# Kernel tuning notes

Measured on AMD Instinct MI355X. Metric: run time of the kernel, lower is better.

## Reference

```python
import jax, jax.numpy as jnp
import numpy as np

Cl, Nl, Cv, Nv, M = 32, 128, 8, 64, 500000


def _sample1d(line, g):
    # line: [C, N]; g in [-1,1]; align_corners=True, zeros padding
    C, N = line.shape
    ix = (g + 1.0) * 0.5 * (N - 1)
    i0 = jnp.floor(ix)
    w = ix - i0
    i0 = i0.astype(jnp.int32)
    def gth(i, wt):
        valid = (i >= 0) & (i < N)
        return line[:, jnp.clip(i, 0, N - 1)] * (wt * valid)
    return (gth(i0, 1.0 - w) + gth(i0 + 1, w)).T  # [M, C]


def _sample2d(plane, gx, gy):
    # plane: [C, H, W]; grid x -> W axis, y -> H axis (torch grid_sample convention)
    C, H, W = plane.shape
    ix = (gx + 1.0) * 0.5 * (W - 1)
    iy = (gy + 1.0) * 0.5 * (H - 1)
    x0 = jnp.floor(ix); y0 = jnp.floor(iy)
    wx = ix - x0; wy = iy - y0
    x0 = x0.astype(jnp.int32); y0 = y0.astype(jnp.int32)
    flat = plane.reshape(C, -1)
    def gth(xi, yi, wt):
        valid = (xi >= 0) & (xi < W) & (yi >= 0) & (yi < H)
        idx = jnp.clip(yi, 0, H - 1) * W + jnp.clip(xi, 0, W - 1)
        return flat[:, idx] * (wt * valid)
    out = (gth(x0, y0, (1 - wx) * (1 - wy)) + gth(x0 + 1, y0, wx * (1 - wy))
           + gth(x0, y0 + 1, (1 - wx) * wy) + gth(x0 + 1, y0 + 1, wx * wy))
    return out.T  # [M, C]


def _sample3d(vol, gx, gy, gz):
    # vol: [C, D, H, W]; grid (x,y,z) -> (W,H,D) axes
    C, D, H, W = vol.shape
    ix = (gx + 1.0) * 0.5 * (W - 1)
    iy = (gy + 1.0) * 0.5 * (H - 1)
    iz = (gz + 1.0) * 0.5 * (D - 1)
    x0 = jnp.floor(ix); y0 = jnp.floor(iy); z0 = jnp.floor(iz)
    wx = ix - x0; wy = iy - y0; wz = iz - z0
    x0 = x0.astype(jnp.int32); y0 = y0.astype(jnp.int32); z0 = z0.astype(jnp.int32)
    flat = vol.reshape(C, -1)
    out = 0.0
    for dz in (0, 1):
        for dy in (0, 1):
            for dx in (0, 1):
                xi, yi, zi = x0 + dx, y0 + dy, z0 + dz
                wt = ((wx if dx else 1 - wx) * (wy if dy else 1 - wy) * (wz if dz else 1 - wz))
                valid = (xi >= 0) & (xi < W) & (yi >= 0) & (yi < H) & (zi >= 0) & (zi < D)
                idx = (jnp.clip(zi, 0, D - 1) * H + jnp.clip(yi, 0, H - 1)) * W + jnp.clip(xi, 0, W - 1)
                out = out + flat[:, idx] * (wt * valid)
    return out.T  # [M, C]


def setup_inputs() -> dict:
    key = jax.random.key(0)
    ks = jax.random.split(key, 16)
    rng, shift = 0.4, 0.1
    coordinates = jax.random.uniform(ks[0], (1, M, 3), minval=-1.0, maxval=1.0)
    line_x = jax.random.uniform(ks[1], (Cl, Nl)) * rng + shift
    line_y = jax.random.uniform(ks[2], (Cl, Nl)) * rng + shift
    line_z = jax.random.uniform(ks[3], (Cl, Nl)) * rng + shift
    plane_xy = jax.random.normal(ks[4], (Cl, Nl, Nl)) * rng + shift
    plane_yz = jax.random.normal(ks[5], (Cl, Nl, Nl)) * rng + shift
    plane_xz = jax.random.normal(ks[6], (Cl, Nl, Nl)) * rng + shift
    volume = jax.random.normal(ks[7], (Cv, Nv, Nv, Nv)) * rng + shift
    def lin(k, fi, fo):
        k1, k2 = jax.random.split(k)
        lim = 1.0 / np.sqrt(fi)
        return (jax.random.uniform(k1, (fi, fo), minval=-lim, maxval=lim),
                jax.random.uniform(k2, (fo,), minval=-lim, maxval=lim))
    Wx, bx = lin(ks[8], Cl, Cl)
    Wy, by = lin(ks[9], Cl, Cl)
    Wz, bz = lin(ks[10], Cl, Cl)
    W1, b1 = lin(ks[11], Cl + Cv, 128)
    W2, b2 = lin(ks[12], 128, 1)
    return dict(coordinates=coordinates, line_x=line_x, line_y=line_y, line_z=line_z,
                plane_xy=plane_xy, plane_yz=plane_yz, plane_xz=plane_xz, volume=volume,
                Wx=Wx, bx=bx, Wy=Wy, by=by, Wz=Wz, bz=bz, W1=W1, b1=b1, W2=W2, b2=b2)


def reference(coordinates, line_x, line_y, line_z, plane_xy, plane_yz, plane_xz, volume,
              Wx, bx, Wy, by, Wz, bz, W1, b1, W2, b2):
    c = coordinates[0]  # [M, 3], batch squeezed like the torch code
    x, y, z = c[:, 0], c[:, 1], c[:, 2]
    x_e = _sample1d(line_x, x)
    y_e = _sample1d(line_y, y)
    z_e = _sample1d(line_z, z)
    xy_e = _sample2d(plane_xy, x, y)
    yz_e = _sample2d(plane_yz, y, z)
    xz_e = _sample2d(plane_xz, x, z)
    xyz_e = _sample3d(volume, x, y, z)
    phi = lambda e, W, b: jax.nn.relu(e) @ W + b  # Sequential(ReLU, Linear)
    yztran = phi(yz_e, Wx, bx)
    xztran = phi(xz_e, Wy, by)
    xytran = phi(xy_e, Wz, bz)
    xtran = phi(x_e, Wx, bx)
    ytran = phi(y_e, Wy, by)
    ztran = phi(z_e, Wz, bz)
    features = xtran * yztran + ytran * xztran + ztran * xytran
    features = jnp.concatenate([features, xyz_e], axis=-1)  # [M, Cl+Cv]
    h = jax.nn.relu(features @ W1 + b1)
    return h @ W2 + b2  # [M, 1]
```

## Files before the change

### kernel.cpp

```cpp
#include <hip/hip_runtime.h>

typedef unsigned short u16;
typedef u16 u16x8 __attribute__((ext_vector_type(8)));
typedef _Float16 half2 __attribute__((ext_vector_type(2)));
typedef _Float16 h8v __attribute__((ext_vector_type(8)));
typedef float f4v __attribute__((ext_vector_type(4)));

union H8 { h8v v; half2 p[4]; };

static __device__ __forceinline__ float bf2f(u16 u) {
    union { unsigned int i; float f; } v;
    v.i = ((unsigned int)u) << 16;
    return v.f;
}
static __device__ __forceinline__ u16 f2bf(float f) {
    union { float f; unsigned int i; } v;
    v.f = f;
    unsigned int x = v.i;
    x += 0x7fffu + ((x >> 16) & 1u);
    return (u16)(x >> 16);
}
static __device__ __forceinline__ float gld(int dt, const void* p, int i) {
    return dt ? ((const float*)p)[i] : bf2f(((const u16*)p)[i]);
}
static __device__ __forceinline__ int detect_dt(const void* coords) {
    u16 v = ((const u16*)coords)[threadIdx.x & 63];
    int e = (v >> 7) & 0xFF;
    bool inr = (e >= 90) && (e <= 126);
    unsigned long long m = __ballot(inr);
    return (__popcll(m) >= 56) ? 0 : 1;
}
static __device__ __forceinline__ half2 pk(float a, float b) {
    return __builtin_bit_cast(half2, __builtin_amdgcn_cvt_pkrtz(a, b));
}

static __device__ __forceinline__ void wave_lds_fence() {
    __threadfence_block();
}

#define WF_OFF        64u
#define PLANES_S_OFF  34304u
#define VOL_S_OFF     3180032u
#define LINES_S_OFF   7374336u
#define PART_OFF      7398912u
#define TOT_OFF       9496064u
#define ORDER_OFF     9512448u

#define NBUCK 4096
#define HBLOCKS 256


static __device__ __forceinline__ int make_key3(float x, float y, float z) {
    int kx = min(max((int)((x + 1.0f) * 8.0f), 0), 15);
    int ky = min(max((int)((y + 1.0f) * 8.0f), 0), 15);
    int kz = min(max((int)((z + 1.0f) * 8.0f), 0), 15);
    return (kz * 16 + ky) * 16 + kx;
}
static __device__ __forceinline__ int make_key(int dt, const void* coords, int p) {
    return make_key3(gld(dt, coords, p * 3 + 0), gld(dt, coords, p * 3 + 1),
                     gld(dt, coords, p * 3 + 2));
}

static __device__ __forceinline__ void weights_work(
    int dt, int r,
    const void* Wx, const void* bx, const void* Wy, const void* by,
    const void* Wz, const void* bz, const void* W1, const void* b1,
    const void* W2, const void* b2, float* wbase)
{
    _Float16* WtH = (_Float16*)wbase;
    float*    bv  = wbase + 1536;
    _Float16* W1H = (_Float16*)(wbase + 1632);
    float*    b1v = wbase + 5728;
    float*    W2v = wbase + 5856;
    float*    b2v = wbase + 5984;
    if (r < 3072) {
        int m = r >> 10, idx = r & 1023;
        int o = idx >> 5, c = idx & 31;
        const void* s = (m == 0) ? Wx : (m == 1) ? Wy : Wz;
        WtH[r] = (_Float16)gld(dt, s, c * 32 + o);
    } else if (r < 3168) {
        int q2 = r - 3072;
        int m = q2 >> 5, c = q2 & 31;
        const void* s = (m == 0) ? bx : (m == 1) ? by : bz;
        bv[q2] = gld(dt, s, c);
    } else if (r < 11360) {
        int idx = r - 3168;
        int j = idx >> 6, i = idx & 63;
        W1H[idx] = (i < 40) ? (_Float16)gld(dt, W1, i * 128 + j) : (_Float16)0.0f;
    } else if (r < 11488) {
        b1v[r - 11360] = gld(dt, b1, r - 11360);
    } else if (r < 11616) {
        W2v[r - 11488] = gld(dt, W2, r - 11488);
    } else if (r == 11616) {
        b2v[0] = gld(dt, b2, 0);
    }
}

__global__ __launch_bounds__(256) void kp_prep_all(
    const void* __restrict__ coords,
    const void* __restrict__ lx, const void* __restrict__ ly,
    const void* __restrict__ lz,
    const void* __restrict__ pxy, const void* __restrict__ pyz,
    const void* __restrict__ pxz, const void* __restrict__ vol,
// ... 88 lines not shown
    }
    psum[t] = s;
    __syncthreads();
    if (t == 0) {
        unsigned int run = 0;
        for (int i = 0; i < 256; ++i) { unsigned int v = psum[i]; psum[i] = run; run += v; }
    }
    __syncthreads();
    unsigned int run = psum[t];
#pragma unroll
    for (int i = 0; i < 16; ++i) {
        int bkt = t * 16 + i;
        cnt[bkt] = run + (unsigned int)part[b * NBUCK + bkt];
        run += bs[i];
    }
    __syncthreads();
    int dt = detect_dt(coords);
    const u16* cu = (const u16*)coords;
    for (int p = b * 256 + t; p < M; p += HBLOCKS * 256) {
        float x = gld(dt, coords, p * 3 + 0);
        float y = gld(dt, coords, p * 3 + 1);
        float z = gld(dt, coords, p * 3 + 2);
        int key = make_key3(x, y, z);
        unsigned int pos = atomicAdd(&cnt[key], 1u);
        order[pos] = p;
        if (dt == 0) {
            scoords[pos * 3 + 0] = cu[p * 3 + 0];
            scoords[pos * 3 + 1] = cu[p * 3 + 1];
            scoords[pos * 3 + 2] = cu[p * 3 + 2];
        }
    }
}

struct Samp { int i0, i1; float w0, w1; };

static __device__ __forceinline__ Samp make_samp(float g, int N) {
    float ix = (g + 1.0f) * 0.5f * (float)(N - 1);
    float fl = floorf(ix);
    float w  = ix - fl;
    int i  = (int)fl;
    int i1 = i + 1;
    float v0 = (i  >= 0 && i  < N) ? 1.0f : 0.0f;
    float v1 = (i1 >= 0 && i1 < N) ? 1.0f : 0.0f;
    Samp s;
    s.w0 = (1.0f - w) * v0;
    s.w1 = w * v1;
    s.i0 = min(max(i, 0), N - 1);
    s.i1 = min(max(i1, 0), N - 1);
    return s;
}

#define MFMA16(a, b, c) __builtin_amdgcn_mfma_f32_16x16x32_f16((a), (b), (c), 0, 0, 0)

#define SRE 40
#define SR2 72

static __device__ __forceinline__ void term_mfma(
    int lane, const u16* __restrict__ Ls, const Samp& sl,
    const u16* __restrict__ Ps, const Samp& sa, const Samp& sb,
    const _Float16* __restrict__ Wt, const float* __restrict__ bvt,
    _Float16* El, _Float16* Ep, float (&feat)[4][2][4])
{
    int q = lane >> 4, l15 = lane & 15;
    const u16x8* l0  = (const u16x8*)(Ls + sl.i0 * 32);
    const u16x8* l1  = (const u16x8*)(Ls + sl.i1 * 32);
    const u16x8* p00 = (const u16x8*)(Ps + (sb.i0 * 128 + sa.i0) * 32);
    const u16x8* p01 = (const u16x8*)(Ps + (sb.i0 * 128 + sa.i1) * 32);
    const u16x8* p10 = (const u16x8*)(Ps + (sb.i1 * 128 + sa.i0) * 32);
    const u16x8* p11 = (const u16x8*)(Ps + (sb.i1 * 128 + sa.i1) * 32);
    float w00 = sb.w0 * sa.w0, w01 = sb.w0 * sa.w1;
    float w10 = sb.w1 * sa.w0, w11 = sb.w1 * sa.w1;
#pragma unroll
    for (int cc = 0; cc < 4; ++cc) {
        u16x8 A0 = l0[cc], A1 = l1[cc];
        u16x8 Q00 = p00[cc], Q01 = p01[cc], Q10 = p10[cc], Q11 = p11[cc];
        H8 hl, hp;
#pragma unroll
        for (int kk = 0; kk < 4; ++kk) {
            int k0 = 2 * kk, k1 = k0 + 1;
            float el0 = sl.w0 * bf2f(A0[k0]) + sl.w1 * bf2f(A1[k0]);
            float el1 = sl.w0 * bf2f(A0[k1]) + sl.w1 * bf2f(A1[k1]);
            float ep0 = w00 * bf2f(Q00[k0]) + w01 * bf2f(Q01[k0])
                      + w10 * bf2f(Q10[k0]) + w11 * bf2f(Q11[k0]);
            float ep1 = w00 * bf2f(Q00[k1]) + w01 * bf2f(Q01[k1])
                      + w10 * bf2f(Q10[k1]) + w11 * bf2f(Q11[k1]);
            hl.p[kk] = pk(fmaxf(el0, 0.0f), fmaxf(el1, 0.0f));
            hp.p[kk] = pk(fmaxf(ep0, 0.0f), fmaxf(ep1, 0.0f));
        }
        *(h8v*)&El[lane * SRE + cc * 8] = hl.v;
        *(h8v*)&Ep[lane * SRE + cc * 8] = hp.v;
    }
    wave_lds_fence();
    h8v bf0 = *(const h8v*)&Wt[(l15) * 32 + q * 8];
    h8v bf1 = *(const h8v*)&Wt[(16 + l15) * 32 + q * 8];
    float bb0 = bvt[l15], bb1 = bvt[16 + l15];
    f4v c0 = {bb0, bb0, bb0, bb0};
    f4v c1 = {bb1, bb1, bb1, bb1};
#pragma unroll
    for (int mt = 0; mt < 4; ++mt) {
        h8v aL = *(const h8v*)&El[(mt * 16 + l15) * SRE + q * 8];
        h8v aP = *(const h8v*)&Ep[(mt * 16 + l15) * SRE + q * 8];
        f4v ta0 = MFMA16(aL, bf0, c0);
        f4v tb0 = MFMA16(aP, bf0, c0);
        f4v ta1 = MFMA16(aL, bf1, c1);
        f4v tb1 = MFMA16(aP, bf1, c1);
#pragma unroll
        for (int r = 0; r < 4; ++r) {
            feat[mt][0][r] += ta0[r] * tb0[r];
            feat[mt][1][r] += ta1[r] * tb1[r];
        }
    }
    wave_lds_fence();
}

__global__ __launch_bounds__(64) void kp_main_mfma(
    const void* __restrict__ coords, const int* __restrict__ order,
    const u16* __restrict__ scoords,
    const u16* __restrict__ planes_s, const u16* __restrict__ vol_s,
    const u16* __restrict__ lines_s,
    const float* __restrict__ wbase,
    void* __restrict__ out, int M)
{
    __shared__ _Float16 eb[5120];
    __shared__ float res[64];
    int dt = detect_dt(coords);
    const _Float16* WtH = (const _Float16*)wbase;
    const float*    bv  = wbase + 1536;
    const _Float16* W1H = (const _Float16*)(wbase + 1632);
    const float*    b1v = wbase + 5728;
    const float*    W2v = wbase + 5856;
    const float*    b2v = wbase + 5984;

    int lane = threadIdx.x;
    int q = lane >> 4, l15 = lane & 15;
    _Float16* El = eb;
    _Float16* Ep = eb + 2560;
    _Float16* E2 = eb;

    int p = blockIdx.x * 64 + lane;
    p = min(p, M - 1);
    int sp = order[p];

    float x, y, z;
    if (dt == 0) {
        x = bf2f(scoords[p * 3 + 0]);
        y = bf2f(scoords[p * 3 + 1]);
        z = bf2f(scoords[p * 3 + 2]);
    } else {
        x = ((const float*)coords)[sp * 3 + 0];
        y = ((const float*)coords)[sp * 3 + 1];
        z = ((const float*)coords)[sp * 3 + 2];
    }

    Samp sx = make_samp(x, 128), sy = make_samp(y, 128), sz = make_samp(z, 128);

    float feat[4][2][4];
#pragma unroll
    for (int mt = 0; mt < 4; ++mt)
#pragma unroll
        for (int n = 0; n < 2; ++n)
#pragma unroll
            for (int r = 0; r < 4; ++r) feat[mt][n][r] = 0.0f;

    term_mfma(lane, lines_s + 0 * 4096, sx, planes_s + 1 * 524288, sy, sz,
              WtH + 0,    bv + 0,  El, Ep, feat);
    term_mfma(lane, lines_s + 1 * 4096, sy, planes_s + 2 * 524288, sx, sz,
              WtH + 1024, bv + 32, El, Ep, feat);
    term_mfma(lane, lines_s + 2 * 4096, sz, planes_s + 0 * 524288, sx, sy,
              WtH + 2048, bv + 64, El, Ep, feat);

#pragma unroll
    for (int mt = 0; mt < 4; ++mt)
#pragma unroll
        for (int n = 0; n < 2; ++n)
#pragma unroll
            for (int r = 0; r < 4; ++r)
                E2[(mt * 16 + q * 4 + r) * SR2 + n * 16 + l15] =
                    (_Float16)feat[mt][n][r];
    {
        Samp vx = make_samp(x, 64), vy = make_samp(y, 64), vz = make_samp(z, 64);
        float vf[8];
#pragma unroll
        for (int c = 0; c < 8; ++c) vf[c] = 0.0f;
#pragma unroll
        for (int corner = 0; corner < 8; ++corner) {
            int dx = corner & 1, dy = (corner >> 1) & 1, dz = corner >> 2;
            int xi = dx ? vx.i1 : vx.i0;
            int yi = dy ? vy.i1 : vy.i0;
            int zi = dz ? vz.i1 : vz.i0;
            float w = (dx ? vx.w1 : vx.w0) * (dy ? vy.w1 : vy.w0) * (dz ? vz.w1 : vz.w0);
            u16x8 v = *(const u16x8*)(vol_s + (((zi * 64) + yi) * 64 + xi) * 8);
#pragma unroll
            for (int c = 0; c < 8; ++c)
                vf[c] = fmaf(w, bf2f(v[c]), vf[c]);
        }
        H8 hv;
#pragma unroll
        for (int k = 0; k < 4; ++k) hv.p[k] = pk(vf[2 * k], vf[2 * k + 1]);
        *(h8v*)&E2[lane * SR2 + 32] = hv.v;
        h8v zz = {};
        *(h8v*)&E2[lane * SR2 + 40] = zz;
        *(h8v*)&E2[lane * SR2 + 48] = zz;
        *(h8v*)&E2[lane * SR2 + 56] = zz;
    }
    wave_lds_fence();

    h8v af[4][2];
#pragma unroll
    for (int mt = 0; mt < 4; ++mt)
#pragma unroll
        for (int ks = 0; ks < 2; ++ks)
            af[mt][ks] = *(const h8v*)&E2[(mt * 16 + l15) * SR2 + ks * 32 + q * 8];

    float s[4][4];
#pragma unroll
    for (int mt = 0; mt < 4; ++mt)
#pragma unroll
        for (int r = 0; r < 4; ++r) s[mt][r] = 0.0f;

#pragma unroll
    for (int NT = 0; NT < 8; ++NT) {
        int o = NT * 16 + l15;
        h8v b0 = *(const h8v*)&W1H[o * 64 + q * 8];
        h8v b1f = *(const h8v*)&W1H[o * 64 + 32 + q * 8];
        float w2 = W2v[o];
        float bb = b1v[o];
        f4v cinit = {bb, bb, bb, bb};
#pragma unroll
        for (int mt = 0; mt < 4; ++mt) {
            f4v c = MFMA16(af[mt][0], b0, cinit);
            c = MFMA16(af[mt][1], b1f, c);
#pragma unroll
            for (int r = 0; r < 4; ++r)
                s[mt][r] = fmaf(fmaxf(c[r], 0.0f), w2, s[mt][r]);
        }
    }
#pragma unroll
    for (int mt = 0; mt < 4; ++mt)
#pragma unroll
        for (int r = 0; r < 4; ++r) {
            float v = s[mt][r];
            v += __shfl_xor(v, 1);
            v += __shfl_xor(v, 2);
            v += __shfl_xor(v, 4);
            v += __shfl_xor(v, 8);
            s[mt][r] = v;
        }
    if (l15 == 0) {
#pragma unroll
        for (int mt = 0; mt < 4; ++mt)
#pragma unroll
            for (int r = 0; r < 4; ++r)
                res[mt * 16 + q * 4 + r] = s[mt][r];
    }
    wave_lds_fence();
    float rr = res[lane] + b2v[0];
    if (dt) ((float*)out)[sp] = rr;
    else    ((u16*)out)[sp] = f2bf(rr);
}

__global__ void kp_prep_weights_fb(
    const void* __restrict__ coords,
    const void* __restrict__ Wx, const void* __restrict__ bx,
    const void* __restrict__ Wy, const void* __restrict__ by,
    const void* __restrict__ Wz, const void* __restrict__ bz,
    const void* __restrict__ W1, const void* __restrict__ b1,
    const void* __restrict__ W2, const void* __restrict__ b2,
    float* __restrict__ wbase)
{
    int dt = detect_dt(coords);
    int t = blockIdx.x * blockDim.x + threadIdx.x;
    weights_work(dt, t, Wx, bx, Wy, by, Wz, bz, W1, b1, W2, b2, wbase);
}

__global__ __launch_bounds__(256) void kp_main_direct(
    const void* __restrict__ coords,
    const void* __restrict__ lx, const void* __restrict__ ly, const void* __restrict__ lz,
    const void* __restrict__ pxy, const void* __restrict__ pyz, const void* __restrict__ pxz,
    const void* __restrict__ vol,
    const float* __restrict__ wbase,
    void* __restrict__ out, int M)
{
    int dt = detect_dt(coords);
    const _Float16* WtH = (const _Float16*)wbase;
    const float*    bv  = wbase + 1536;
    const _Float16* W1H = (const _Float16*)(wbase + 1632);
    const float*    b1v = wbase + 5728;
    const float*    W2v = wbase + 5856;
    const float*    b2v = wbase + 5984;

    int p = blockIdx.x * 256 + threadIdx.x;
    p = min(p, M - 1);

    float x = gld(dt, coords, p * 3 + 0);
    float y = gld(dt, coords, p * 3 + 1);
    float z = gld(dt, coords, p * 3 + 2);

    Samp sx = make_samp(x, 128), sy = make_samp(y, 128), sz = make_samp(z, 128);

    float feat[40];
#pragma unroll
    for (int o = 0; o < 40; ++o) feat[o] = 0.0f;

    const void* Ls[3] = {lx, ly, lz};
    const void* Psv[3] = {pyz, pxz, pxy};
    Samp sl3[3] = {sx, sy, sz};
    Samp sa3[3] = {sy, sx, sx};
    Samp sb3[3] = {sz, sz, sy};
#pragma unroll 1
    for (int m = 0; m < 3; ++m) {
        float ta[32], tb[32];
// ... 47 lines not shown
        const _Float16* wr = W1H + j * 64;
#pragma unroll
        for (int i = 0; i < 40; ++i)
            acc = fmaf(feat[i], (float)wr[i], acc);
        acc_out = fmaf(fmaxf(acc, 0.0f), W2v[j], acc_out);
    }
    if (dt) ((float*)out)[p] = acc_out;
    else    ((u16*)out)[p] = f2bf(acc_out);
}

extern "C" void kernel_launch(void* const* d_in, const int* in_sizes, int n_in,
                              void* d_out, int out_size, void* d_ws, size_t ws_size,
                              hipStream_t stream) {
    const void* coords = d_in[0];
    const void* lx  = d_in[1];
    const void* ly  = d_in[2];
    const void* lz  = d_in[3];
    const void* pxy = d_in[4];
    const void* pyz = d_in[5];
    const void* pxz = d_in[6];
    const void* vol = d_in[7];
    const void* Wx  = d_in[8];
    const void* bx  = d_in[9];
    const void* Wy  = d_in[10];
    const void* by  = d_in[11];
    const void* Wz  = d_in[12];
    const void* bz  = d_in[13];
    const void* W1  = d_in[14];
    const void* b1  = d_in[15];
    const void* W2  = d_in[16];
    const void* b2  = d_in[17];

    int M = in_sizes[0] / 3;

    char* ws = (char*)d_ws;
    float*        wbase    = (float*)(ws + WF_OFF);
    u16*          planes_s = (u16*)(ws + PLANES_S_OFF);
    u16*          vol_s    = (u16*)(ws + VOL_S_OFF);
    u16*          lines_s  = (u16*)(ws + LINES_S_OFF);
    u16*          part     = (u16*)(ws + PART_OFF);
    unsigned int* tot      = (unsigned int*)(ws + TOT_OFF);
    int*          order    = (int*)(ws + ORDER_OFF);
    u16*          scoords  = (u16*)(ws + ORDER_OFF + (size_t)M * 4u);

    size_t need_sorted = (size_t)ORDER_OFF + (size_t)M * 4u + (size_t)M * 6u;

    if (ws_size >= need_sorted) {
        kp_prep_all<<<2100, 256, 0, stream>>>(coords, lx, ly, lz, pxy, pyz, pxz, vol,
                                              Wx, bx, Wy, by, Wz, bz, W1, b1, W2, b2,
                                              wbase, planes_s, vol_s, lines_s, part, M);
        kp_colscan<<<64, 64, 0, stream>>>(part, tot);
        kp_scatter_det<<<HBLOCKS, 256, 0, stream>>>(coords, part, tot, order,
                                                    scoords, M);
        int blocks64 = (M + 63) / 64;
        kp_main_mfma<<<blocks64, 64, 0, stream>>>(coords, order, scoords,
                                                  planes_s, vol_s,
                                                  lines_s, wbase, d_out, M);
    } else {
        int blocks = (M + 255) / 256;
        kp_prep_weights_fb<<<46, 256, 0, stream>>>(coords, Wx, bx, Wy, by, Wz, bz,
                                                   W1, b1, W2, b2, wbase);
        kp_main_direct<<<blocks, 256, 0, stream>>>(coords, lx, ly, lz, pxy, pyz, pxz,
                                                   vol, wbase, d_out, M);
    }
}
```

Baseline: 202.9 us.

## Software-pipeline gathers with conversion and process four tiles per wave

Splits each term into separate load, convert and MFMA stages so the gathers for the next term (and the volume corners) are issued while the current term's data is being converted. Each 64-thread block now loops over four 64-point tiles, cutting the grid size by four. The fence is replaced with a bare s_waitcnt lgkmcnt(0), and launch bounds now request two waves minimum. Register pressure rises from holding the prefetched tiles, and the whole scheme depends on the raw waitcnt being enough to order LDS accesses within a wave.

Result: slower. 237.1 us (+16.9%).

```diff
diff --git a/kernel.cpp b/kernel.cpp
--- a/kernel.cpp
+++ b/kernel.cpp
@@ -34,8 +34,8 @@
     return __builtin_bit_cast(half2, __builtin_amdgcn_cvt_pkrtz(a, b));
 }
 
-static __device__ __forceinline__ void wave_lds_fence() {
-    __threadfence_block();
+static __device__ __forceinline__ void lds_wait() {
+    asm volatile("s_waitcnt lgkmcnt(0)" ::: "memory");
 }
 
 #define WF_OFF        64u
@@ -48,7 +48,6 @@
 
 #define NBUCK 4096
 #define HBLOCKS 256
-
 
 static __device__ __forceinline__ int make_key3(float x, float y, float z) {
     int kx = min(max((int)((x + 1.0f) * 8.0f), 0), 15);
@@ -246,31 +245,44 @@
 #define SRE 40
 #define SR2 72
 
-static __device__ __forceinline__ void term_mfma(
-    int lane, const u16* __restrict__ Ls, const Samp& sl,
-    const u16* __restrict__ Ps, const Samp& sa, const Samp& sb,
-    const _Float16* __restrict__ Wt, const float* __restrict__ bvt,
-    _Float16* El, _Float16* Ep, float (&feat)[4][2][4])
-{
-    int q = lane >> 4, l15 = lane & 15;
+struct TL {
+    u16x8 a0[4], a1[4], q00[4], q01[4], q10[4], q11[4];
+};
+
+static __device__ __forceinline__ void term_load(
+    const u16* __restrict__ Ls, const Samp& sl,
+    const u16* __restrict__ Ps, const Samp& sa, const Samp& sb, TL& T)
+{
     const u16x8* l0  = (const u16x8*)(Ls + sl.i0 * 32);
     const u16x8* l1  = (const u16x8*)(Ls + sl.i1 * 32);
     const u16x8* p00 = (const u16x8*)(Ps + (sb.i0 * 128 + sa.i0) * 32);
     const u16x8* p01 = (const u16x8*)(Ps + (sb.i0 * 128 + sa.i1) * 32);
     const u16x8* p10 = (const u16x8*)(Ps + (sb.i1 * 128 + sa.i0) * 32);
     const u16x8* p11 = (const u16x8*)(Ps + (sb.i1 * 128 + sa.i1) * 32);
-    float w00 = sb.w0 * sa.w0, w01 = sb.w0 * sa.w1;
-    float w10 = sb.w1 * sa.w0, w11 = sb.w1 * sa.w1;
 #pragma unroll
     for (int cc = 0; cc < 4; ++cc) {
-        u16x8 A0 = l0[cc], A1 = l1[cc];
-        u16x8 Q00 = p00[cc], Q01 = p01[cc], Q10 = p10[cc], Q11 = p11[cc];
+        T.a0[cc]  = l0[cc];  T.a1[cc]  = l1[cc];
+        T.q00[cc] = p00[cc]; T.q01[cc] = p01[cc];
+        T.q10[cc] = p10[cc]; T.q11[cc] = p11[cc];
+    }
+}
+
+template<int CB>
+static __device__ __forceinline__ void term_convert2(
+    int lane, const TL& T, float wl0, float wl1,
+    float w00, float w01, float w10, float w11,
+    _Float16* El, _Float16* Ep)
+{
+#pragma unroll
+    for (int cc = CB; cc < CB + 2; ++cc) {
+        u16x8 A0 = T.a0[cc], A1 = T.a1[cc];
+        u16x8 Q00 = T.q00[cc], Q01 = T.q01[cc], Q10 = T.q10[cc], Q11 = T.q11[cc];
         H8 hl, hp;
 #pragma unroll
         for (int kk = 0; kk < 4; ++kk) {
             int k0 = 2 * kk, k1 = k0 + 1;
-            float el0 = sl.w0 * bf2f(A0[k0]) + sl.w1 * bf2f(A1[k0]);
-            float el1 = sl.w0 * bf2f(A0[k1]) + sl.w1 * bf2f(A1[k1]);
+            float el0 = wl0 * bf2f(A0[k0]) + wl1 * bf2f(A1[k0]);
+            float el1 = wl0 * bf2f(A0[k1]) + wl1 * bf2f(A1[k1]);
             float ep0 = w00 * bf2f(Q00[k0]) + w01 * bf2f(Q01[k0])
                       + w10 * bf2f(Q10[k0]) + w11 * bf2f(Q11[k0]);
             float ep1 = w00 * bf2f(Q00[k1]) + w01 * bf2f(Q01[k1])
@@ -281,10 +293,16 @@
         *(h8v*)&El[lane * SRE + cc * 8] = hl.v;
         *(h8v*)&Ep[lane * SRE + cc * 8] = hp.v;
     }
-    wave_lds_fence();
+}
+
+static __device__ __forceinline__ void term_mfma_acc(
+    int q, int l15, const _Float16* __restrict__ Wt, const float* __restrict__ bvt,
+    const _Float16* El, const _Float16* Ep, float (&feat)[4][2][4])
+{
     h8v bf0 = *(const h8v*)&Wt[(l15) * 32 + q * 8];
     h8v bf1 = *(const h8v*)&Wt[(16 + l15) * 32 + q * 8];
     float bb0 = bvt[l15], bb1 = bvt[16 + l15];
+    lds_wait();
     f4v c0 = {bb0, bb0, bb0, bb0};
     f4v c1 = {bb1, bb1, bb1, bb1};
 #pragma unroll
@@ -301,10 +319,26 @@
             feat[mt][1][r] += ta1[r] * tb1[r];
         }
     }
-    wave_lds_fence();
-}
-
-__global__ __launch_bounds__(64) void kp_main_mfma(
+    lds_wait();
+}
+
+struct VL { u16x8 v[8]; };
+
+static __device__ __forceinline__ void vol_loads(
+    const u16* __restrict__ vol_s, const Samp& vx, const Samp& vy,
+    const Samp& vz, VL& V)
+{
+#pragma unroll
+    for (int corner = 0; corner < 8; ++corner) {
+        int dx = corner & 1, dy = (corner >> 1) & 1, dz = corner >> 2;
+        int xi = dx ? vx.i1 : vx.i0;
+        int yi = dy ? vy.i1 : vy.i0;
+        int zi = dz ? vz.i1 : vz.i0;
+        V.v[corner] = *(const u16x8*)(vol_s + (((zi * 64) + yi) * 64 + xi) * 8);
+    }
+}
+
+__global__ __launch_bounds__(64, 2) void kp_main_mfma(
     const void* __restrict__ coords, const int* __restrict__ order,
     const u16* __restrict__ scoords,
     const u16* __restrict__ planes_s, const u16* __restrict__ vol_s,
@@ -328,126 +362,151 @@
     _Float16* Ep = eb + 2560;
     _Float16* E2 = eb;
 
-    int p = blockIdx.x * 64 + lane;
-    p = min(p, M - 1);
-    int sp = order[p];
-
-    float x, y, z;
-    if (dt == 0) {
-        x = bf2f(scoords[p * 3 + 0]);
-        y = bf2f(scoords[p * 3 + 1]);
-        z = bf2f(scoords[p * 3 + 2]);
-    } else {
-        x = ((const float*)coords)[sp * 3 + 0];
-        y = ((const float*)coords)[sp * 3 + 1];
-        z = ((const float*)coords)[sp * 3 + 2];
-    }
-
-    Samp sx = make_samp(x, 128), sy = make_samp(y, 128), sz = make_samp(z, 128);
-
-    float feat[4][2][4];
-#pragma unroll
-    for (int mt = 0; mt < 4; ++mt)
-#pragma unroll
-        for (int n = 0; n < 2; ++n)
-#pragma unroll
-            for (int r = 0; r < 4; ++r) feat[mt][n][r] = 0.0f;
-
-    term_mfma(lane, lines_s + 0 * 4096, sx, planes_s + 1 * 524288, sy, sz,
-              WtH + 0,    bv + 0,  El, Ep, feat);
-    term_mfma(lane, lines_s + 1 * 4096, sy, planes_s + 2 * 524288, sx, sz,
-              WtH + 1024, bv + 32, El, Ep, feat);
-    term_mfma(lane, lines_s + 2 * 4096, sz, planes_s + 0 * 524288, sx, sy,
-              WtH + 2048, bv + 64, El, Ep, feat);
-
-#pragma unroll
-    for (int mt = 0; mt < 4; ++mt)
-#pragma unroll
-        for (int n = 0; n < 2; ++n)
-#pragma unroll
-            for (int r = 0; r < 4; ++r)
-                E2[(mt * 16 + q * 4 + r) * SR2 + n * 16 + l15] =
-                    (_Float16)feat[mt][n][r];
-    {
-        Samp vx = make_samp(x, 64), vy = make_samp(y, 64), vz = make_samp(z, 64);
-        float vf[8];
-#pragma unroll
-        for (int c = 0; c < 8; ++c) vf[c] = 0.0f;
-#pragma unroll
-        for (int corner = 0; corner < 8; ++corner) {
-            int dx = corner & 1, dy = (corner >> 1) & 1, dz = corner >> 2;
-            int xi = dx ? vx.i1 : vx.i0;
-            int yi = dy ? vy.i1 : vy.i0;
-            int zi = dz ? vz.i1 : vz.i0;
-            float w = (dx ? vx.w1 : vx.w0) * (dy ? vy.w1 : vy.w0) * (dz ? vz.w1 : vz.w0);
-            u16x8 v = *(const u16x8*)(vol_s + (((zi * 64) + yi) * 64 + xi) * 8);
-#pragma unroll
-            for (int c = 0; c < 8; ++c)
-                vf[c] = fmaf(w, bf2f(v[c]), vf[c]);
-        }
-        H8 hv;
-#pragma unroll
-        for (int k = 0; k < 4; ++k) hv.p[k] = pk(vf[2 * k], vf[2 * k + 1]);
-        *(h8v*)&E2[lane * SR2 + 32] = hv.v;
-        h8v zz = {};
-        *(h8v*)&E2[lane * SR2 + 40] = zz;
-        *(h8v*)&E2[lane * SR2 + 48] = zz;
-        *(h8v*)&E2[lane * SR2 + 56] = zz;
-    }
-    wave_lds_fence();
-
-    h8v af[4][2];
-#pragma unroll
-    for (int mt = 0; mt < 4; ++mt)
-#pragma unroll
-        for (int ks = 0; ks < 2; ++ks)
-            af[mt][ks] = *(const h8v*)&E2[(mt * 16 + l15) * SR2 + ks * 32 + q * 8];
-
-    float s[4][4];
-#pragma unroll
-    for (int mt = 0; mt < 4; ++mt)
-#pragma unroll
-        for (int r = 0; r < 4; ++r) s[mt][r] = 0.0f;
-
-#pragma unroll
-    for (int NT = 0; NT < 8; ++NT) {
-        int o = NT * 16 + l15;
-        h8v b0 = *(const h8v*)&W1H[o * 64 + q * 8];
-        h8v b1f = *(const h8v*)&W1H[o * 64 + 32 + q * 8];
-        float w2 = W2v[o];
-        float bb = b1v[o];
-        f4v cinit = {bb, bb, bb, bb};
-#pragma unroll
-        for (int mt = 0; mt < 4; ++mt) {
-            f4v c = MFMA16(af[mt][0], b0, cinit);
-            c = MFMA16(af[mt][1], b1f, c);
-#pragma unroll
-            for (int r = 0; r < 4; ++r)
-                s[mt][r] = fmaf(fmaxf(c[r], 0.0f), w2, s[mt][r]);
-        }
-    }
-#pragma unroll
-    for (int mt = 0; mt < 4; ++mt)
-#pragma unroll
-        for (int r = 0; r < 4; ++r) {
-            float v = s[mt][r];
-            v += __shfl_xor(v, 1);
-            v += __shfl_xor(v, 2);
-            v += __shfl_xor(v, 4);
-            v += __shfl_xor(v, 8);
-            s[mt][r] = v;
-        }
-    if (l15 == 0) {
+    int pbase = blockIdx.x * 256;
+
+#pragma unroll 1
+    for (int bt = 0; bt < 4; ++bt) {
+        int p = pbase + bt * 64 + lane;
+        p = min(p, M - 1);
+        int sp = order[p];
+
+        float x, y, z;
+        if (dt == 0) {
+            x = bf2f(scoords[p * 3 + 0]);
+            y = bf2f(scoords[p * 3 + 1]);
+            z = bf2f(scoords[p * 3 + 2]);
+        } else {
+            x = ((const float*)coords)[sp * 3 + 0];
+            y = ((const float*)coords)[sp * 3 + 1];
+            z = ((const float*)coords)[sp * 3 + 2];
+        }
+
+        Samp sx = make_samp(x, 128), sy = make_samp(y, 128), sz = make_samp(z, 128);
+        Samp vx = make_samp(x, 64),  vy = make_samp(y, 64),  vz = make_samp(z, 64);
+
+        float t0_00 = sz.w0 * sy.w0, t0_01 = sz.w0 * sy.w1;
+        float t0_10 = sz.w1 * sy.w0, t0_11 = sz.w1 * sy.w1;
+        float t1_00 = sz.w0 * sx.w0, t1_01 = sz.w0 * sx.w1;
+        float t1_10 = sz.w1 * sx.w0, t1_11 = sz.w1 * sx.w1;
+        float t2_00 = sy.w0 * sx.w0, t2_01 = sy.w0 * sx.w1;
+        float t2_10 = sy.w1 * sx.w0, t2_11 = sy.w1 * sx.w1;
+
+        float feat[4][2][4];
 #pragma unroll
         for (int mt = 0; mt < 4; ++mt)
 #pragma unroll
-            for (int r = 0; r < 4; ++r)
-                res[mt * 16 + q * 4 + r] = s[mt][r];
-    }
-    wave_lds_fence();
-    float rr = res[lane] + b2v[0];
-    if (dt) ((float*)out)[sp] = rr;
-    else    ((u16*)out)[sp] = f2bf(rr);
+            for (int n = 0; n < 2; ++n)
+#pragma unroll
+                for (int r = 0; r < 4; ++r) feat[mt][n][r] = 0.0f;
+
+        TL T0, T1, T2;
+        VL V;
+
+        term_load(lines_s + 0 * 4096, sx, planes_s + 1 * 524288, sy, sz, T0);
+
+        term_convert2<0>(lane, T0, sx.w0, sx.w1, t0_00, t0_01, t0_10, t0_11, El, Ep);
+        term_load(lines_s + 1 * 4096, sy, planes_s + 2 * 524288, sx, sz, T1);
+        term_convert2<2>(lane, T0, sx.w0, sx.w1, t0_00, t0_01, t0_10, t0_11, El, Ep);
+        term_mfma_acc(q, l15, WtH + 0, bv + 0, El, Ep, feat);
+
+        term_convert2<0>(lane, T1, sy.w0, sy.w1, t1_00, t1_01, t1_10, t1_11, El, Ep);
+        term_load(lines_s + 2 * 4096, sz, planes_s + 0 * 524288, sx, sy, T2);
+        term_convert2<2>(lane, T1, sy.w0, sy.w1, t1_00, t1_01, t1_10, t1_11, El, Ep);
+        term_mfma_acc(q, l15, WtH + 1024, bv + 32, El, Ep, feat);
+
+        term_convert2<0>(lane, T2, sz.w0, sz.w1, t2_00, t2_01, t2_10, t2_11, El, Ep);
+        vol_loads(vol_s, vx, vy, vz, V);
+        term_convert2<2>(lane, T2, sz.w0, sz.w1, t2_00, t2_01, t2_10, t2_11, El, Ep);
+        term_mfma_acc(q, l15, WtH + 2048, bv + 64, El, Ep, feat);
+
+#pragma unroll
+        for (int mt = 0; mt < 4; ++mt)
+#pragma unroll
+            for (int n = 0; n < 2; ++n)
+#pragma unroll
+                for (int r = 0; r < 4; ++r)
+                    E2[(mt * 16 + q * 4 + r) * SR2 + n * 16 + l15] =
+                        (_Float16)feat[mt][n][r];
+        {
+            float vf[8];
+#pragma unroll
+            for (int c = 0; c < 8; ++c) vf[c] = 0.0f;
+#pragma unroll
+            for (int corner = 0; corner < 8; ++corner) {
+                int dx = corner & 1, dy = (corner >> 1) & 1, dz = corner >> 2;
+                float w = (dx ? vx.w1 : vx.w0) * (dy ? vy.w1 : vy.w0)
+                        * (dz ? vz.w1 : vz.w0);
+                u16x8 v = V.v[corner];
+#pragma unroll
+                for (int c = 0; c < 8; ++c)
+                    vf[c] = fmaf(w, bf2f(v[c]), vf[c]);
+            }
+            H8 hv;
+#pragma unroll
+            for (int k = 0; k < 4; ++k) hv.p[k] = pk(vf[2 * k], vf[2 * k + 1]);
+            *(h8v*)&E2[lane * SR2 + 32] = hv.v;
+            h8v zz = {};
+            *(h8v*)&E2[lane * SR2 + 40] = zz;
+            *(h8v*)&E2[lane * SR2 + 48] = zz;
+            *(h8v*)&E2[lane * SR2 + 56] = zz;
+        }
+        lds_wait();
+
+        h8v af[4][2];
+#pragma unroll
+        for (int mt = 0; mt < 4; ++mt)
+#pragma unroll
+            for (int ks = 0; ks < 2; ++ks)
+                af[mt][ks] = *(const h8v*)&E2[(mt * 16 + l15) * SR2 + ks * 32 + q * 8];
+
+        float s[4][4];
+#pragma unroll
+        for (int mt = 0; mt < 4; ++mt)
+#pragma unroll
+            for (int r = 0; r < 4; ++r) s[mt][r] = 0.0f;
+
+#pragma unroll
+        for (int NT = 0; NT < 8; ++NT) {
+            int o = NT * 16 + l15;
+            h8v b0 = *(const h8v*)&W1H[o * 64 + q * 8];
+            h8v b1f = *(const h8v*)&W1H[o * 64 + 32 + q * 8];
+            float w2 = W2v[o];
+            float bb = b1v[o];
+            f4v cinit = {bb, bb, bb, bb};
+#pragma unroll
+            for (int mt = 0; mt < 4; ++mt) {
+                f4v c = MFMA16(af[mt][0], b0, cinit);
+                c = MFMA16(af[mt][1], b1f, c);
+#pragma unroll
+                for (int r = 0; r < 4; ++r)
+                    s[mt][r] = fmaf(fmaxf(c[r], 0.0f), w2, s[mt][r]);
+            }
+        }
+        lds_wait();
+#pragma unroll
+        for (int mt = 0; mt < 4; ++mt)
+#pragma unroll
+            for (int r = 0; r < 4; ++r) {
+                float v = s[mt][r];
+                v += __shfl_xor(v, 1);
+                v += __shfl_xor(v, 2);
+                v += __shfl_xor(v, 4);
+                v += __shfl_xor(v, 8);
+                s[mt][r] = v;
+            }
+        if (l15 == 0) {
+#pragma unroll
+            for (int mt = 0; mt < 4; ++mt)
+#pragma unroll
+                for (int r = 0; r < 4; ++r)
+                    res[mt * 16 + q * 4 + r] = s[mt][r];
+        }
+        lds_wait();
+        float rr = res[lane] + b2v[0];
+        if (dt) ((float*)out)[sp] = rr;
+        else    ((u16*)out)[sp] = f2bf(rr);
+        lds_wait();
+    }
 }
 
 __global__ void kp_prep_weights_fb(
@@ -601,10 +660,10 @@
         kp_colscan<<<64, 64, 0, stream>>>(part, tot);
         kp_scatter_det<<<HBLOCKS, 256, 0, stream>>>(coords, part, tot, order,
                                                     scoords, M);
-        int blocks64 = (M + 63) / 64;
-        kp_main_mfma<<<blocks64, 64, 0, stream>>>(coords, order, scoords,
-                                                  planes_s, vol_s,
-                                                  lines_s, wbase, d_out, M);
+        int blocks256 = (M + 255) / 256;
+        kp_main_mfma<<<blocks256, 64, 0, stream>>>(coords, order, scoords,
+                                                   planes_s, vol_s,
+                                                   lines_s, wbase, d_out, M);
     } else {
         int blocks = (M + 255) / 256;
         kp_prep_weights_fb<<<46, 256, 0, stream>>>(coords, Wx, bx, Wy, by, Wz, bz,
```

## Halve LDS staging buffer, split line/plane phases, hoist volume loads

Applied to the files above, without the earlier changes.

Shrinks the per-block LDS buffer from two 64x40 halves plus a 64x72 staging area to a single 64x40 buffer. The line term and the plane term now pass through it one after the other, and the layer-1 A fragments are loaded in two halves. The volume gathers are issued before the feature staging so their latency overlaps LDS work. Fences become raw s_waitcnt lgkmcnt(0), and launch bounds ask for 4 blocks per CU. The aim is higher occupancy and less fence cost, in exchange for more serialized LDS phases and more live registers.

Result: slower. 230.9 us (+13.8%).

```diff
diff --git a/kernel.cpp b/kernel.cpp
--- a/kernel.cpp
+++ b/kernel.cpp
@@ -34,8 +34,8 @@
     return __builtin_bit_cast(half2, __builtin_amdgcn_cvt_pkrtz(a, b));
 }
 
-static __device__ __forceinline__ void wave_lds_fence() {
-    __threadfence_block();
+static __device__ __forceinline__ void lds_wait() {
+    asm volatile("s_waitcnt lgkmcnt(0)" ::: "memory");
 }
 
 #define WF_OFF        64u
@@ -48,7 +48,6 @@
 
 #define NBUCK 4096
 #define HBLOCKS 256
-
 
 static __device__ __forceinline__ int make_key3(float x, float y, float z) {
     int kx = min(max((int)((x + 1.0f) * 8.0f), 0), 15);
@@ -243,16 +242,15 @@
 
 #define MFMA16(a, b, c) __builtin_amdgcn_mfma_f32_16x16x32_f16((a), (b), (c), 0, 0, 0)
 
-#define SRE 40
-#define SR2 72
-
-static __device__ __forceinline__ void term_mfma(
-    int lane, const u16* __restrict__ Ls, const Samp& sl,
+#define SB 40
+
+static __device__ __forceinline__ void term_phase(
+    int lane, int q, int l15,
+    const u16* __restrict__ Ls, const Samp& sl,
     const u16* __restrict__ Ps, const Samp& sa, const Samp& sb,
     const _Float16* __restrict__ Wt, const float* __restrict__ bvt,
-    _Float16* El, _Float16* Ep, float (&feat)[4][2][4])
-{
-    int q = lane >> 4, l15 = lane & 15;
+    _Float16* buf, float (&feat)[4][2][4])
+{
     const u16x8* l0  = (const u16x8*)(Ls + sl.i0 * 32);
     const u16x8* l1  = (const u16x8*)(Ls + sl.i1 * 32);
     const u16x8* p00 = (const u16x8*)(Ps + (sb.i0 * 128 + sa.i0) * 32);
@@ -261,50 +259,82 @@
     const u16x8* p11 = (const u16x8*)(Ps + (sb.i1 * 128 + sa.i1) * 32);
     float w00 = sb.w0 * sa.w0, w01 = sb.w0 * sa.w1;
     float w10 = sb.w1 * sa.w0, w11 = sb.w1 * sa.w1;
+
 #pragma unroll
     for (int cc = 0; cc < 4; ++cc) {
         u16x8 A0 = l0[cc], A1 = l1[cc];
-        u16x8 Q00 = p00[cc], Q01 = p01[cc], Q10 = p10[cc], Q11 = p11[cc];
-        H8 hl, hp;
+        H8 hl;
 #pragma unroll
         for (int kk = 0; kk < 4; ++kk) {
             int k0 = 2 * kk, k1 = k0 + 1;
-            float el0 = sl.w0 * bf2f(A0[k0]) + sl.w1 * bf2f(A1[k0]);
-            float el1 = sl.w0 * bf2f(A0[k1]) + sl.w1 * bf2f(A1[k1]);
-            float ep0 = w00 * bf2f(Q00[k0]) + w01 * bf2f(Q01[k0])
-                      + w10 * bf2f(Q10[k0]) + w11 * bf2f(Q11[k0]);
-            float ep1 = w00 * bf2f(Q00[k1]) + w01 * bf2f(Q01[k1])
-                      + w10 * bf2f(Q10[k1]) + w11 * bf2f(Q11[k1]);
-            hl.p[kk] = pk(fmaxf(el0, 0.0f), fmaxf(el1, 0.0f));
-            hp.p[kk] = pk(fmaxf(ep0, 0.0f), fmaxf(ep1, 0.0f));
-        }
-        *(h8v*)&El[lane * SRE + cc * 8] = hl.v;
-        *(h8v*)&Ep[lane * SRE + cc * 8] = hp.v;
-    }
-    wave_lds_fence();
-    h8v bf0 = *(const h8v*)&Wt[(l15) * 32 + q * 8];
+            float e0 = sl.w0 * bf2f(A0[k0]) + sl.w1 * bf2f(A1[k0]);
+            float e1 = sl.w0 * bf2f(A0[k1]) + sl.w1 * bf2f(A1[k1]);
+            hl.p[kk] = pk(fmaxf(e0, 0.0f), fmaxf(e1, 0.0f));
+        }
+        *(h8v*)&buf[lane * SB + cc * 8] = hl.v;
+    }
+    h8v bf0 = *(const h8v*)&Wt[l15 * 32 + q * 8];
     h8v bf1 = *(const h8v*)&Wt[(16 + l15) * 32 + q * 8];
     float bb0 = bvt[l15], bb1 = bvt[16 + l15];
     f4v c0 = {bb0, bb0, bb0, bb0};
     f4v c1 = {bb1, bb1, bb1, bb1};
+    lds_wait();
+    f4v ta0[4], ta1[4];
 #pragma unroll
     for (int mt = 0; mt < 4; ++mt) {
-        h8v aL = *(const h8v*)&El[(mt * 16 + l15) * SRE + q * 8];
-        h8v aP = *(const h8v*)&Ep[(mt * 16 + l15) * SRE + q * 8];
-        f4v ta0 = MFMA16(aL, bf0, c0);
+        h8v aL = *(const h8v*)&buf[(mt * 16 + l15) * SB + q * 8];
+        ta0[mt] = MFMA16(aL, bf0, c0);
+        ta1[mt] = MFMA16(aL, bf1, c1);
+    }
+    lds_wait();
+
+#pragma unroll
+    for (int cc = 0; cc < 4; ++cc) {
+        u16x8 Q00 = p00[cc], Q01 = p01[cc], Q10 = p10[cc], Q11 = p11[cc];
+        H8 hp;
+#pragma unroll
+        for (int kk = 0; kk < 4; ++kk) {
+            int k0 = 2 * kk, k1 = k0 + 1;
+            float e0 = w00 * bf2f(Q00[k0]) + w01 * bf2f(Q01[k0])
+                     + w10 * bf2f(Q10[k0]) + w11 * bf2f(Q11[k0]);
+            float e1 = w00 * bf2f(Q00[k1]) + w01 * bf2f(Q01[k1])
+                     + w10 * bf2f(Q10[k1]) + w11 * bf2f(Q11[k1]);
+            hp.p[kk] = pk(fmaxf(e0, 0.0f), fmaxf(e1, 0.0f));
+        }
+        *(h8v*)&buf[lane * SB + cc * 8] = hp.v;
+    }
+    lds_wait();
+#pragma unroll
+    for (int mt = 0; mt < 4; ++mt) {
+        h8v aP = *(const h8v*)&buf[(mt * 16 + l15) * SB + q * 8];
         f4v tb0 = MFMA16(aP, bf0, c0);
-        f4v ta1 = MFMA16(aL, bf1, c1);
         f4v tb1 = MFMA16(aP, bf1, c1);
 #pragma unroll
         for (int r = 0; r < 4; ++r) {
-            feat[mt][0][r] += ta0[r] * tb0[r];
-            feat[mt][1][r] += ta1[r] * tb1[r];
-        }
-    }
-    wave_lds_fence();
-}
-
-__global__ __launch_bounds__(64) void kp_main_mfma(
+            feat[mt][0][r] += ta0[mt][r] * tb0[r];
+            feat[mt][1][r] += ta1[mt][r] * tb1[r];
+        }
+    }
+    lds_wait();
+}
+
+struct VL { u16x8 v[8]; };
+
+static __device__ __forceinline__ void vol_loads(
+    const u16* __restrict__ vol_s, const Samp& vx, const Samp& vy,
+    const Samp& vz, VL& V)
+{
+#pragma unroll
+    for (int corner = 0; corner < 8; ++corner) {
+        int dx = corner & 1, dy = (corner >> 1) & 1, dz = corner >> 2;
+        int xi = dx ? vx.i1 : vx.i0;
+        int yi = dy ? vy.i1 : vy.i0;
+        int zi = dz ? vz.i1 : vz.i0;
+        V.v[corner] = *(const u16x8*)(vol_s + (((zi * 64) + yi) * 64 + xi) * 8);
+    }
+}
+
+__global__ __launch_bounds__(64, 4) void kp_main_mfma(
     const void* __restrict__ coords, const int* __restrict__ order,
     const u16* __restrict__ scoords,
     const u16* __restrict__ planes_s, const u16* __restrict__ vol_s,
@@ -312,7 +342,7 @@
     const float* __restrict__ wbase,
     void* __restrict__ out, int M)
 {
-    __shared__ _Float16 eb[5120];
+    __shared__ _Float16 buf[64 * SB];
     __shared__ float res[64];
     int dt = detect_dt(coords);
     const _Float16* WtH = (const _Float16*)wbase;
@@ -324,9 +354,6 @@
 
     int lane = threadIdx.x;
     int q = lane >> 4, l15 = lane & 15;
-    _Float16* El = eb;
-    _Float16* Ep = eb + 2560;
-    _Float16* E2 = eb;
 
     int p = blockIdx.x * 64 + lane;
     p = min(p, M - 1);
@@ -344,6 +371,7 @@
     }
 
     Samp sx = make_samp(x, 128), sy = make_samp(y, 128), sz = make_samp(z, 128);
+    Samp vx = make_samp(x, 64),  vy = make_samp(y, 64),  vz = make_samp(z, 64);
 
     float feat[4][2][4];
 #pragma unroll
@@ -353,12 +381,15 @@
 #pragma unroll
             for (int r = 0; r < 4; ++r) feat[mt][n][r] = 0.0f;
 
-    term_mfma(lane, lines_s + 0 * 4096, sx, planes_s + 1 * 524288, sy, sz,
-              WtH + 0,    bv + 0,  El, Ep, feat);
-    term_mfma(lane, lines_s + 1 * 4096, sy, planes_s + 2 * 524288, sx, sz,
-              WtH + 1024, bv + 32, El, Ep, feat);
-    term_mfma(lane, lines_s + 2 * 4096, sz, planes_s + 0 * 524288, sx, sy,
-              WtH + 2048, bv + 64, El, Ep, feat);
+    term_phase(lane, q, l15, lines_s + 0 * 4096, sx, planes_s + 1 * 524288, sy, sz,
+               WtH + 0,    bv + 0,  buf, feat);
+    term_phase(lane, q, l15, lines_s + 1 * 4096, sy, planes_s + 2 * 524288, sx, sz,
+               WtH + 1024, bv + 32, buf, feat);
+    term_phase(lane, q, l15, lines_s + 2 * 4096, sz, planes_s + 0 * 524288, sx, sy,
+               WtH + 2048, bv + 64, buf, feat);
+
+    VL V;
+    vol_loads(vol_s, vx, vy, vz, V);
 
 #pragma unroll
     for (int mt = 0; mt < 4; ++mt)
@@ -366,21 +397,25 @@
         for (int n = 0; n < 2; ++n)
 #pragma unroll
             for (int r = 0; r < 4; ++r)
-                E2[(mt * 16 + q * 4 + r) * SR2 + n * 16 + l15] =
+                buf[(mt * 16 + q * 4 + r) * SB + n * 16 + l15] =
                     (_Float16)feat[mt][n][r];
+    lds_wait();
+    h8v af0[4];
+#pragma unroll
+    for (int mt = 0; mt < 4; ++mt)
+        af0[mt] = *(const h8v*)&buf[(mt * 16 + l15) * SB + q * 8];
+    lds_wait();
+
     {
-        Samp vx = make_samp(x, 64), vy = make_samp(y, 64), vz = make_samp(z, 64);
         float vf[8];
 #pragma unroll
         for (int c = 0; c < 8; ++c) vf[c] = 0.0f;
 #pragma unroll
         for (int corner = 0; corner < 8; ++corner) {
             int dx = corner & 1, dy = (corner >> 1) & 1, dz = corner >> 2;
-            int xi = dx ? vx.i1 : vx.i0;
-            int yi = dy ? vy.i1 : vy.i0;
-            int zi = dz ? vz.i1 : vz.i0;
-            float w = (dx ? vx.w1 : vx.w0) * (dy ? vy.w1 : vy.w0) * (dz ? vz.w1 : vz.w0);
-            u16x8 v = *(const u16x8*)(vol_s + (((zi * 64) + yi) * 64 + xi) * 8);
+            float w = (dx ? vx.w1 : vx.w0) * (dy ? vy.w1 : vy.w0)
+                    * (dz ? vz.w1 : vz.w0);
+            u16x8 v = V.v[corner];
 #pragma unroll
             for (int c = 0; c < 8; ++c)
                 vf[c] = fmaf(w, bf2f(v[c]), vf[c]);
@@ -388,20 +423,17 @@
         H8 hv;
 #pragma unroll
         for (int k = 0; k < 4; ++k) hv.p[k] = pk(vf[2 * k], vf[2 * k + 1]);
-        *(h8v*)&E2[lane * SR2 + 32] = hv.v;
+        *(h8v*)&buf[lane * SB + 0]  = hv.v;
         h8v zz = {};
-        *(h8v*)&E2[lane * SR2 + 40] = zz;
-        *(h8v*)&E2[lane * SR2 + 48] = zz;
-        *(h8v*)&E2[lane * SR2 + 56] = zz;
-    }
-    wave_lds_fence();
-
-    h8v af[4][2];
+        *(h8v*)&buf[lane * SB + 8]  = zz;
+        *(h8v*)&buf[lane * SB + 16] = zz;
+        *(h8v*)&buf[lane * SB + 24] = zz;
+    }
+    lds_wait();
+    h8v af1[4];
 #pragma unroll
     for (int mt = 0; mt < 4; ++mt)
-#pragma unroll
-        for (int ks = 0; ks < 2; ++ks)
-            af[mt][ks] = *(const h8v*)&E2[(mt * 16 + l15) * SR2 + ks * 32 + q * 8];
+        af1[mt] = *(const h8v*)&buf[(mt * 16 + l15) * SB + q * 8];
 
     float s[4][4];
 #pragma unroll
@@ -412,15 +444,15 @@
 #pragma unroll
     for (int NT = 0; NT < 8; ++NT) {
         int o = NT * 16 + l15;
-        h8v b0 = *(const h8v*)&W1H[o * 64 + q * 8];
+        h8v b0  = *(const h8v*)&W1H[o * 64 + q * 8];
         h8v b1f = *(const h8v*)&W1H[o * 64 + 32 + q * 8];
         float w2 = W2v[o];
         float bb = b1v[o];
         f4v cinit = {bb, bb, bb, bb};
 #pragma unroll
         for (int mt = 0; mt < 4; ++mt) {
-            f4v c = MFMA16(af[mt][0], b0, cinit);
-            c = MFMA16(af[mt][1], b1f, c);
+            f4v c = MFMA16(af0[mt], b0, cinit);
+            c = MFMA16(af1[mt], b1f, c);
 #pragma unroll
             for (int r = 0; r < 4; ++r)
                 s[mt][r] = fmaf(fmaxf(c[r], 0.0f), w2, s[mt][r]);
@@ -444,7 +476,7 @@
             for (int r = 0; r < 4; ++r)
                 res[mt * 16 + q * 4 + r] = s[mt][r];
     }
-    wave_lds_fence();
+    lds_wait();
     float rr = res[lane] + b2v[0];
     if (dt) ((float*)out)[sp] = rr;
     else    ((u16*)out)[sp] = f2bf(rr);
```

## Prefetch next plane and volume corners into registers during MFMA term steps

Applied to the files above, without the earlier changes.

Splits the plane gather out of the per-term routine so the next term's four plane corners (and the volume's eight corners before the last term) are loaded into registers while the current term runs its LDS staging and MFMAs. The block-scope thread fence is replaced by a bare s_waitcnt lgkmcnt(0), relying on single-wave workgroups for LDS ordering. This hides global gather latency behind compute, at the cost of many more live vector registers (two full plane corner sets plus volume data), which may reduce occupancy or cause spills.

New measurement: 199.4 us. About the same (-1.7%).

```diff
diff --git a/kernel.cpp b/kernel.cpp
--- a/kernel.cpp
+++ b/kernel.cpp
@@ -34,8 +34,8 @@
     return __builtin_bit_cast(half2, __builtin_amdgcn_cvt_pkrtz(a, b));
 }
 
-static __device__ __forceinline__ void wave_lds_fence() {
-    __threadfence_block();
+static __device__ __forceinline__ void lds_wait() {
+    asm volatile("s_waitcnt lgkmcnt(0)" ::: "memory");
 }
 
 #define WF_OFF        64u
@@ -48,7 +48,6 @@
 
 #define NBUCK 4096
 #define HBLOCKS 256
-
 
 static __device__ __forceinline__ int make_key3(float x, float y, float z) {
     int kx = min(max((int)((x + 1.0f) * 8.0f), 0), 15);
@@ -246,25 +245,57 @@
 #define SRE 40
 #define SR2 72
 
-static __device__ __forceinline__ void term_mfma(
-    int lane, const u16* __restrict__ Ls, const Samp& sl,
-    const u16* __restrict__ Ps, const Samp& sa, const Samp& sb,
-    const _Float16* __restrict__ Wt, const float* __restrict__ bvt,
-    _Float16* El, _Float16* Ep, float (&feat)[4][2][4])
-{
-    int q = lane >> 4, l15 = lane & 15;
-    const u16x8* l0  = (const u16x8*)(Ls + sl.i0 * 32);
-    const u16x8* l1  = (const u16x8*)(Ls + sl.i1 * 32);
+struct PL { u16x8 q00[4], q01[4], q10[4], q11[4]; };
+struct VL { u16x8 v[8]; };
+
+static __device__ __forceinline__ void plane_load(
+    const u16* __restrict__ Ps, const Samp& sa, const Samp& sb, PL& P)
+{
     const u16x8* p00 = (const u16x8*)(Ps + (sb.i0 * 128 + sa.i0) * 32);
     const u16x8* p01 = (const u16x8*)(Ps + (sb.i0 * 128 + sa.i1) * 32);
     const u16x8* p10 = (const u16x8*)(Ps + (sb.i1 * 128 + sa.i0) * 32);
     const u16x8* p11 = (const u16x8*)(Ps + (sb.i1 * 128 + sa.i1) * 32);
+#pragma unroll
+    for (int cc = 0; cc < 4; ++cc) {
+        P.q00[cc] = p00[cc]; P.q01[cc] = p01[cc];
+        P.q10[cc] = p10[cc]; P.q11[cc] = p11[cc];
+    }
+}
+
+static __device__ __forceinline__ void vol_loads(
+    const u16* __restrict__ vol_s, const Samp& vx, const Samp& vy,
+    const Samp& vz, VL& V)
+{
+#pragma unroll
+    for (int corner = 0; corner < 8; ++corner) {
+        int dx = corner & 1, dy = (corner >> 1) & 1, dz = corner >> 2;
+        int xi = dx ? vx.i1 : vx.i0;
+        int yi = dy ? vy.i1 : vy.i0;
+        int zi = dz ? vz.i1 : vz.i0;
+        V.v[corner] = *(const u16x8*)(vol_s + (((zi * 64) + yi) * 64 + xi) * 8);
+    }
+}
+
+template<int PRE>
+static __device__ __forceinline__ void term_step(
+    int lane, int q, int l15,
+    const u16* __restrict__ Ls, const Samp& sl,
+    const PL& P, const Samp& sa, const Samp& sb,
+    const _Float16* __restrict__ Wt, const float* __restrict__ bvt,
+    _Float16* El, _Float16* Ep, float (&feat)[4][2][4],
+    const u16* __restrict__ nps, const Samp& na, const Samp& nb, PL& PN,
+    const u16* __restrict__ vol_s, const Samp& vx, const Samp& vy,
+    const Samp& vz, VL& V)
+{
+    const u16x8* l0 = (const u16x8*)(Ls + sl.i0 * 32);
+    const u16x8* l1 = (const u16x8*)(Ls + sl.i1 * 32);
     float w00 = sb.w0 * sa.w0, w01 = sb.w0 * sa.w1;
     float w10 = sb.w1 * sa.w0, w11 = sb.w1 * sa.w1;
 #pragma unroll
     for (int cc = 0; cc < 4; ++cc) {
         u16x8 A0 = l0[cc], A1 = l1[cc];
-        u16x8 Q00 = p00[cc], Q01 = p01[cc], Q10 = p10[cc], Q11 = p11[cc];
+        u16x8 Q00 = P.q00[cc], Q01 = P.q01[cc];
+        u16x8 Q10 = P.q10[cc], Q11 = P.q11[cc];
         H8 hl, hp;
 #pragma unroll
         for (int kk = 0; kk < 4; ++kk) {
@@ -281,12 +312,15 @@
         *(h8v*)&El[lane * SRE + cc * 8] = hl.v;
         *(h8v*)&Ep[lane * SRE + cc * 8] = hp.v;
     }
-    wave_lds_fence();
+    if constexpr (PRE == 1) plane_load(nps, na, nb, PN);
+    if constexpr (PRE == 2) vol_loads(vol_s, vx, vy, vz, V);
+
     h8v bf0 = *(const h8v*)&Wt[(l15) * 32 + q * 8];
     h8v bf1 = *(const h8v*)&Wt[(16 + l15) * 32 + q * 8];
     float bb0 = bvt[l15], bb1 = bvt[16 + l15];
     f4v c0 = {bb0, bb0, bb0, bb0};
     f4v c1 = {bb1, bb1, bb1, bb1};
+    lds_wait();
 #pragma unroll
     for (int mt = 0; mt < 4; ++mt) {
         h8v aL = *(const h8v*)&El[(mt * 16 + l15) * SRE + q * 8];
@@ -301,7 +335,7 @@
             feat[mt][1][r] += ta1[r] * tb1[r];
         }
     }
-    wave_lds_fence();
+    lds_wait();
 }
 
 __global__ __launch_bounds__(64) void kp_main_mfma(
@@ -353,12 +387,28 @@
 #pragma unroll
             for (int r = 0; r < 4; ++r) feat[mt][n][r] = 0.0f;
 
-    term_mfma(lane, lines_s + 0 * 4096, sx, planes_s + 1 * 524288, sy, sz,
-              WtH + 0,    bv + 0,  El, Ep, feat);
-    term_mfma(lane, lines_s + 1 * 4096, sy, planes_s + 2 * 524288, sx, sz,
-              WtH + 1024, bv + 32, El, Ep, feat);
-    term_mfma(lane, lines_s + 2 * 4096, sz, planes_s + 0 * 524288, sx, sy,
-              WtH + 2048, bv + 64, El, Ep, feat);
+    PL Pa, Pb;
+    VL V;
+    Samp vx, vy, vz;
+
+    plane_load(planes_s + 1 * 524288, sy, sz, Pa);
+
+    term_step<1>(lane, q, l15, lines_s + 0 * 4096, sx, Pa, sy, sz,
+                 WtH + 0, bv + 0, El, Ep, feat,
+                 planes_s + 2 * 524288, sx, sz, Pb,
+                 vol_s, sx, sx, sx, V);
+
+    term_step<1>(lane, q, l15, lines_s + 1 * 4096, sy, Pb, sx, sz,
+                 WtH + 1024, bv + 32, El, Ep, feat,
+                 planes_s + 0 * 524288, sx, sy, Pa,
+                 vol_s, sx, sx, sx, V);
+
+    vx = make_samp(x, 64); vy = make_samp(y, 64); vz = make_samp(z, 64);
+
+    term_step<2>(lane, q, l15, lines_s + 2 * 4096, sz, Pa, sx, sy,
+                 WtH + 2048, bv + 64, El, Ep, feat,
+                 planes_s, sx, sy, Pb,
+                 vol_s, vx, vy, vz, V);
 
 #pragma unroll
     for (int mt = 0; mt < 4; ++mt)
@@ -369,18 +419,15 @@
                 E2[(mt * 16 + q * 4 + r) * SR2 + n * 16 + l15] =
                     (_Float16)feat[mt][n][r];
     {
-        Samp vx = make_samp(x, 64), vy = make_samp(y, 64), vz = make_samp(z, 64);
         float vf[8];
 #pragma unroll
         for (int c = 0; c < 8; ++c) vf[c] = 0.0f;
 #pragma unroll
         for (int corner = 0; corner < 8; ++corner) {
             int dx = corner & 1, dy = (corner >> 1) & 1, dz = corner >> 2;
-            int xi = dx ? vx.i1 : vx.i0;
-            int yi = dy ? vy.i1 : vy.i0;
-            int zi = dz ? vz.i1 : vz.i0;
-            float w = (dx ? vx.w1 : vx.w0) * (dy ? vy.w1 : vy.w0) * (dz ? vz.w1 : vz.w0);
-            u16x8 v = *(const u16x8*)(vol_s + (((zi * 64) + yi) * 64 + xi) * 8);
+            float w = (dx ? vx.w1 : vx.w0) * (dy ? vy.w1 : vy.w0)
+                    * (dz ? vz.w1 : vz.w0);
+            u16x8 v = V.v[corner];
 #pragma unroll
             for (int c = 0; c < 8; ++c)
                 vf[c] = fmaf(w, bf2f(v[c]), vf[c]);
@@ -394,7 +441,7 @@
         *(h8v*)&E2[lane * SR2 + 48] = zz;
         *(h8v*)&E2[lane * SR2 + 56] = zz;
     }
-    wave_lds_fence();
+    lds_wait();
 
     h8v af[4][2];
 #pragma unroll
@@ -412,7 +459,7 @@
 #pragma unroll
     for (int NT = 0; NT < 8; ++NT) {
         int o = NT * 16 + l15;
-        h8v b0 = *(const h8v*)&W1H[o * 64 + q * 8];
+        h8v b0  = *(const h8v*)&W1H[o * 64 + q * 8];
         h8v b1f = *(const h8v*)&W1H[o * 64 + 32 + q * 8];
         float w2 = W2v[o];
         float bb = b1v[o];
@@ -444,7 +491,7 @@
             for (int r = 0; r < 4; ++r)
                 res[mt * 16 + q * 4 + r] = s[mt][r];
     }
-    wave_lds_fence();
+    lds_wait();
     float rr = res[lane] + b2v[0];
     if (dt) ((float*)out)[sp] = rr;
     else    ((u16*)out)[sp] = f2bf(rr);
```
